# Performance work log

Measured on AMD Instinct MI355X. Metric: run time of the kernel, lower is better.

The kernel has to match this reference:

```python
import jax, jax.numpy as jnp
import numpy as np
import math

D = 1024
H = 16
B = 4
N = 2048


def setup_inputs() -> dict:
    key = jax.random.key(0)
    ks = jax.random.split(key, 10)
    scale_qkv = 0.01
    def kaiming_uniform(k, shape, scale):
        # attenuated_kaiming_uniform_: fan_in = shape[1], gain for leaky_relu a=sqrt(5)
        fan_in = shape[1]
        gain = math.sqrt(2.0 / (1 + 5.0))
        bound = math.sqrt(3.0) * gain * scale / math.sqrt(fan_in)
        return jax.random.uniform(k, shape, jnp.float32, -bound, bound)
    return {
        "x_q": jax.random.normal(ks[0], (B, N, D), jnp.float32),
        "x_kv": jax.random.normal(ks[1], (B, N, D), jnp.float32),
        "Wq": kaiming_uniform(ks[2], (D, D), scale_qkv),
        "bq": jnp.zeros((D,), jnp.float32),
        "Wk": kaiming_uniform(ks[3], (D, D), scale_qkv),
        "bk": jnp.zeros((D,), jnp.float32),
        "Wv": kaiming_uniform(ks[4], (D, D), scale_qkv),
        "bv": jnp.zeros((D,), jnp.float32),
        "Wo": kaiming_uniform(ks[5], (D, D), 1.0),
        "bo": jnp.zeros((D,), jnp.float32),
    }


def reference(x_q, x_kv, Wq, bq, Wk, bk, Wv, bv, Wo, bo):
    bs, n, d = x_q.shape
    hd = d // H  # head dim
    # torch Linear: y = x @ W^T + b
    q = x_q @ Wq.T + bq
    k = x_kv @ Wk.T + bk
    v = x_kv @ Wv.T + bv
    # reshape to [bs, H, n, hd]
    q = q.reshape(bs, n, H, hd).transpose(0, 2, 1, 3)
    k = k.reshape(bs, n, H, hd).transpose(0, 2, 1, 3)
    v = v.reshape(bs, n, H, hd).transpose(0, 2, 1, 3)
    scores = jnp.einsum("bhqd,bhkd->bhqk", q, k) / math.sqrt(hd)
    seq_ids = jnp.arange(n)
    causal = (seq_ids[None, :] <= seq_ids[:, None]).astype(scores.dtype)  # [n, n]
    scores = scores + (1.0 - causal) * -10000.0
    probs = jax.nn.softmax(scores, axis=-1)
    out = jnp.einsum("bhqk,bhkd->bhqd", probs, v)
    out = out.transpose(0, 2, 1, 3).reshape(bs, n, d)
    return out @ Wo.T + bo
```

## Files before the change

### kernel.cpp

```cpp
#include <hip/hip_runtime.h>

typedef unsigned short u16;
typedef unsigned int u32;
typedef __attribute__((ext_vector_type(8))) short short8;
typedef __attribute__((ext_vector_type(4))) float f32x4;
typedef __attribute__((ext_vector_type(16))) float f32x16;
typedef __attribute__((ext_vector_type(4))) unsigned u32x4;

#define ASYNC_CP16(gsrc, ldst) \
  __builtin_amdgcn_global_load_lds((__attribute__((address_space(1))) void*)(gsrc), \
                                   (__attribute__((address_space(3))) void*)(ldst), 16, 0, 0)

static __device__ __forceinline__ u16 f2bf(float f) {
  u32 u = __builtin_bit_cast(u32, f);
  u = u + 0x7fffu + ((u >> 16) & 1u);
  return (u16)(u >> 16);
}
static __device__ __forceinline__ u32 pk2(float a, float b) {
  return (u32)f2bf(a) | ((u32)f2bf(b) << 16);
}
static __device__ __forceinline__ u32 cvtpk(float lo, float hi) {
  u32 r;
  asm("v_cvt_pk_bf16_f32 %0, %1, %2" : "=v"(r) : "v"(lo), "v"(hi));
  return r;
}
static __device__ __forceinline__ void plswap(u32 &a, u32 &b) {
  asm("v_permlane32_swap_b32 %0, %1" : "+v"(a), "+v"(b));
}

__global__ __launch_bounds__(256) void convert_all(
    const float* __restrict__ xq, const float* __restrict__ xkv,
    const float* __restrict__ wq, const float* __restrict__ wk,
    const float* __restrict__ wv, const float* __restrict__ wo,
    u16* __restrict__ dst)
{
  long i = ((long)blockIdx.x * 256 + threadIdx.x) * 4;
  const float* s; long o;
  if      (i < 8388608)  { s = xq;  o = i; }
  else if (i < 16777216) { s = xkv; o = i - 8388608; }
  else if (i < 17825792) { s = wq;  o = i - 16777216; }
  else if (i < 18874368) { s = wk;  o = i - 17825792; }
  else if (i < 19922944) { s = wv;  o = i - 18874368; }
  else                   { s = wo;  o = i - 19922944; }
  float4 v = *(const float4*)(s + o);
  uint2 pkv; pkv.x = pk2(v.x, v.y); pkv.y = pk2(v.z, v.w);
  *(uint2*)(dst + i) = pkv;
}

template<int EPI>
__global__ __launch_bounds__(256)
void gemm_k(const u16* __restrict__ Axq, const u16* __restrict__ Axkv,
            const u16* __restrict__ W0, const u16* __restrict__ W1, const u16* __restrict__ W2,
            const float* __restrict__ b0, const float* __restrict__ b1, const float* __restrict__ b2,
            u16* __restrict__ Qo, u16* __restrict__ Ko, u16* __restrict__ Vo,
            float* __restrict__ Fo)
{
  __shared__ u16 lsa[2][128*32];
  __shared__ u16 lsb[2][128*32];
  const int tid = threadIdx.x;
  const int w = tid >> 6, lane = tid & 63;
  const int wr = w >> 1, wc = w & 1;
  const int bm = blockIdx.x, bn = blockIdx.y, z = blockIdx.z;
  const int l15 = lane & 15, l4 = lane >> 4;

  const u16* A; const u16* W; const float* bias;
  if (EPI == 0) {
    A    = (z == 0) ? Axq : Axkv;
    W    = (z == 0) ? W0 : (z == 1) ? W1 : W2;
    bias = (z == 0) ? b0 : (z == 1) ? b1 : b2;
  } else {
    A = Axq; W = W0; bias = b0;
  }
  const u16* Ag = A + (long)bm*128*1024;
  const u16* Wg = W + (long)bn*128*1024;

  f32x4 acc[4][4];
#pragma unroll
  for (int i = 0; i < 4; ++i)
#pragma unroll
    for (int j = 0; j < 4; ++j)
      acc[i][j] = (f32x4){0.f,0.f,0.f,0.f};

#pragma unroll
  for (int c = 0; c < 2; ++c) {
    int tp = c*256 + tid;
    int row = tp >> 2, col = (tp & 3) * 8;
    ASYNC_CP16(Ag + (long)row*1024 + col, &lsa[0][tp*8]);
    ASYNC_CP16(Wg + (long)row*1024 + col, &lsb[0][tp*8]);
  }

  for (int t = 0; t < 32; ++t) {
    const int cur = t & 1;
    if (t < 31) {
      const int k0 = (t + 1) * 32;
#pragma unroll
      for (int c = 0; c < 2; ++c) {
        int tp = c*256 + tid;
        int row = tp >> 2, col = (tp & 3) * 8;
        ASYNC_CP16(Ag + (long)row*1024 + k0 + col, &lsa[cur^1][tp*8]);
        ASYNC_CP16(Wg + (long)row*1024 + k0 + col, &lsb[cur^1][tp*8]);
      }
      asm volatile("s_waitcnt vmcnt(4)" ::: "memory");
    } else {
      asm volatile("s_waitcnt vmcnt(0)" ::: "memory");
    }
    __builtin_amdgcn_s_barrier();

    short8 af[4], bfr[4];
#pragma unroll
    for (int i = 0; i < 4; ++i)
      af[i] = *(const short8*)&lsa[cur][(wr*64 + i*16 + l15)*32 + l4*8];
#pragma unroll
    for (int j = 0; j < 4; ++j)
      bfr[j] = *(const short8*)&lsb[cur][(wc*64 + j*16 + l15)*32 + l4*8];
#pragma unroll
    for (int i = 0; i < 4; ++i)
#pragma unroll
      for (int j = 0; j < 4; ++j)
        acc[i][j] = __builtin_amdgcn_mfma_f32_16x16x32_bf16(af[i], bfr[j], acc[i][j], 0, 0, 0);

    asm volatile("" ::: "memory");
    __builtin_amdgcn_s_barrier();
  }

#pragma unroll
  for (int j = 0; j < 4; ++j) {
    const int colg = bn*128 + wc*64 + j*16 + l15;
    const float bb = bias[colg];
#pragma unroll
    for (int i = 0; i < 4; ++i) {
      const int rowg = bm*128 + wr*64 + i*16 + l4*4;
      if (EPI == 1) {
#pragma unroll
        for (int r = 0; r < 4; ++r)
          Fo[(long)(rowg + r)*1024 + colg] = acc[i][j][r] + bb;
      } else {
        const int b  = rowg >> 11, n0 = rowg & 2047;
        const int h  = colg >> 6,  c  = colg & 63;
        const int bh = b*16 + h;
        const long hb = (long)bh*131072 + (long)(n0 >> 7)*8192;
        if (z == 0) {
#pragma unroll
          for (int r = 0; r < 4; ++r)
            Qo[((long)bh*2048 + n0 + r)*64 + c] = f2bf((acc[i][j][r] + bb) * 0.18033688f);
        } else if (z == 1) {
          const long base = hb + (long)(c >> 3)*1024 + (n0 & 127)*8 + (c & 7);
#pragma unroll
          for (int r = 0; r < 4; ++r)
            Ko[base + r*8] = f2bf(acc[i][j][r] + bb);
        } else {
          const long base = hb + (long)((n0 & 127) >> 3)*512 + (long)c*8 + (n0 & 7);
          uint2 pkv;
          pkv.x = pk2(acc[i][j][0] + bb, acc[i][j][1] + bb);
          pkv.y = pk2(acc[i][j][2] + bb, acc[i][j][3] + bb);
          *(uint2*)(Vo + base) = pkv;
        }
      }
    }
  }
}

__global__ __launch_bounds__(512, 4)
void attn_k(const u16* __restrict__ Q, const u16* __restrict__ K,
            const u16* __restrict__ V, u16* __restrict__ AO)
{
  __shared__ u16 lk[2][8192];
  __shared__ u16 lv[2][8192];
  const int tid = threadIdx.x;
  const int w = tid >> 6, lane = tid & 63;
  const int l31 = lane & 31, l5 = lane >> 5;
  const int wq = w & 3, hh = w >> 2;
  const int qt = (gridDim.x - 1) - blockIdx.x;
  const int bh = blockIdx.y;
  const int q0 = qt*128;
  const int qg = q0 + wq*32 + l31;
  const u16* Qh = Q + (long)bh*131072;
  const u16* Kh = K + (long)bh*131072;
  const u16* Vh = V + (long)bh*131072;

  short8 qf[4];
#pragma unroll
  for (int ks = 0; ks < 4; ++ks)
    qf[ks] = *(const short8*)&Qh[(long)qg*64 + ks*16 + l5*8];

  f32x16 o0 = (f32x16)0.0f;
  f32x16 o1 = (f32x16)0.0f;
  float rsum = 0.f;

  const int koff = l5*2048 + l31*16;
  const int voff = l5*1024 + l31*16;
  const int ktmax = qt;

#pragma unroll
  for (int c = 0; c < 2; ++c) {
    int tp = c*512 + tid;
    ASYNC_CP16(Kh + tp*8, &lk[0][tp*8]);
    ASYNC_CP16(Vh + tp*8, &lv[0][tp*8]);
  }

  for (int kt = 0; kt <= ktmax; ++kt) {
    const int cur = kt & 1;
    if (kt < ktmax) {
      const long off = (long)(kt + 1)*8192;
#pragma unroll
      for (int c = 0; c < 2; ++c) {
        int tp = c*512 + tid;
        ASYNC_CP16(Kh + off + tp*8, &lk[cur^1][tp*8]);
        ASYNC_CP16(Vh + off + tp*8, &lv[cur^1][tp*8]);
      }
      asm volatile("s_waitcnt vmcnt(4)" ::: "memory");
    } else {
      asm volatile("s_waitcnt vmcnt(0)" ::: "memory");
    }
    __builtin_amdgcn_s_barrier();

    const char* lkc = (const char*)lk + cur*16384;
    const char* lvc = (const char*)lv + cur*16384;

    const bool active = !(kt == ktmax && hh*64 > wq*32 + 31);
    if (active) {
      short8 pf[4];
#pragma unroll
      for (int sbl = 0; sbl < 2; ++sbl) {
        f32x16 sa = (f32x16)0.0f;
#pragma unroll
        for (int ks = 0; ks < 4; ++ks) {
          short8 kf = *(const short8*)(lkc + koff + ks*4096 + (hh*2 + sbl)*512);
          sa = __builtin_amdgcn_mfma_f32_32x32x16_bf16(kf, qf[ks], sa, 0, 0, 0);
        }
        if (kt == ktmax) {
          const int kb = kt*128 + hh*64 + sbl*32 + 4*l5;
#pragma unroll
          for (int g = 0; g < 4; ++g)
#pragma unroll
            for (int rr = 0; rr < 4; ++rr)
              if (kb + 8*g + rr > qg) sa[4*g + rr] = -1e30f;
        }
        float p[16];
#pragma unroll
        for (int r = 0; r < 16; ++r) p[r] = __builtin_amdgcn_exp2f(sa[r]);
#pragma unroll
        for (int g = 0; g < 4; ++g)
          rsum += (p[4*g] + p[4*g+1]) + (p[4*g+2] + p[4*g+3]);
        u32 cc[4][2];
#pragma unroll
        for (int g = 0; g < 4; ++g) {
          cc[g][0] = cvtpk(p[4*g],   p[4*g+1]);
          cc[g][1] = cvtpk(p[4*g+2], p[4*g+3]);
        }
        plswap(cc[0][0], cc[1][0]); plswap(cc[0][1], cc[1][1]);
        plswap(cc[2][0], cc[3][0]); plswap(cc[2][1], cc[3][1]);
        u32x4 pw0 = {cc[0][0], cc[0][1], cc[1][0], cc[1][1]};
        u32x4 pw1 = {cc[2][0], cc[2][1], cc[3][0], cc[3][1]};
        pf[sbl*2]     = __builtin_bit_cast(short8, pw0);
        pf[sbl*2 + 1] = __builtin_bit_cast(short8, pw1);
      }
#pragma unroll
      for (int j = 0; j < 4; ++j) {
        const char* vb = lvc + voff + (hh*4 + j)*2048;
        short8 vf0 = *(const short8*)(vb);
        o0 = __builtin_amdgcn_mfma_f32_32x32x16_bf16(vf0, pf[j], o0, 0, 0, 0);
        short8 vf1 = *(const short8*)(vb + 512);
        o1 = __builtin_amdgcn_mfma_f32_32x32x16_bf16(vf1, pf[j], o1, 0, 0, 0);
      }
    }

    asm volatile("" ::: "memory");
    __builtin_amdgcn_s_barrier();
  }

  __syncthreads();
  float* exf = (float*)&lk[0][0];
  float* rxf = (float*)&lv[0][0];
  const int sw = lane & 7;
  float* xb = exf + wq*2048 + lane*32;

  if (hh == 1) {
#pragma unroll
    for (int c = 0; c < 4; ++c) {
      f32x4 v; v[0]=o0[c*4]; v[1]=o0[c*4+1]; v[2]=o0[c*4+2]; v[3]=o0[c*4+3];
      *(f32x4*)(xb + ((c ^ sw)*4)) = v;
    }
#pragma unroll
    for (int c = 0; c < 4; ++c) {
      f32x4 v; v[0]=o1[c*4]; v[1]=o1[c*4+1]; v[2]=o1[c*4+2]; v[3]=o1[c*4+3];
      *(f32x4*)(xb + (((c+4) ^ sw)*4)) = v;
    }
    rxf[wq*64 + lane] = rsum;
  }
  __syncthreads();
  if (hh == 0) {
    float rt = rsum + rxf[wq*64 + lane];
    rt += __shfl_xor(rt, 32, 64);
    const float inv = 1.0f / rt;
#pragma unroll
    for (int c = 0; c < 4; ++c) {
      f32x4 v = *(const f32x4*)(xb + ((c ^ sw)*4));
      o0[c*4] += v[0]; o0[c*4+1] += v[1]; o0[c*4+2] += v[2]; o0[c*4+3] += v[3];
    }
#pragma unroll
    for (int c = 0; c < 4; ++c) {
      f32x4 v = *(const f32x4*)(xb + (((c+4) ^ sw)*4));
      o1[c*4] += v[0]; o1[c*4+1] += v[1]; o1[c*4+2] += v[2]; o1[c*4+3] += v[3];
    }
    const int b = bh >> 4, h = bh & 15;
    const long tok = (long)b*2048 + qg;
    u16* dst = AO + tok*1024 + h*64;
#pragma unroll
    for (int g = 0; g < 4; ++g) {
      uint2 pkv;
      pkv.x = pk2(o0[4*g]*inv,   o0[4*g+1]*inv);
      pkv.y = pk2(o0[4*g+2]*inv, o0[4*g+3]*inv);
      *(uint2*)(dst + 8*g + 4*l5) = pkv;
    }
#pragma unroll
    for (int g = 0; g < 4; ++g) {
      uint2 pkv;
      pkv.x = pk2(o1[4*g]*inv,   o1[4*g+1]*inv);
      pkv.y = pk2(o1[4*g+2]*inv, o1[4*g+3]*inv);
      *(uint2*)(dst + 32 + 8*g + 4*l5) = pkv;
    }
  }
}

extern "C" void kernel_launch(void* const* d_in, const int* in_sizes, int n_in,
                              void* d_out, int out_size, void* d_ws, size_t ws_size,
                              hipStream_t stream)
{
  const float* xq  = (const float*)d_in[0];
  const float* xkv = (const float*)d_in[1];
  const float* Wq  = (const float*)d_in[2];
  const float* bq  = (const float*)d_in[3];
  const float* Wk  = (const float*)d_in[4];
  const float* bk  = (const float*)d_in[5];
  const float* Wv  = (const float*)d_in[6];
  const float* bv  = (const float*)d_in[7];
  const float* Wo  = (const float*)d_in[8];
  const float* bo  = (const float*)d_in[9];

  u16* ws    = (u16*)d_ws;
  u16* xq_b  = ws;
  u16* xkv_b = xq_b  + (1l<<23);
  u16* wq_b  = xkv_b + (1l<<23);
  u16* wk_b  = wq_b  + (1l<<20);
  u16* wv_b  = wk_b  + (1l<<20);
  u16* wo_b  = wv_b  + (1l<<20);
  u16* Qb    = wo_b  + (1l<<20);
  u16* Kb    = Qb    + (1l<<23);
  u16* Vb    = Kb    + (1l<<23);
  u16* Ab    = Vb    + (1l<<23);

  convert_all<<<20480, 256, 0, stream>>>(xq, xkv, Wq, Wk, Wv, Wo, ws);
  gemm_k<0><<<dim3(64,8,3), 256, 0, stream>>>(xq_b, xkv_b, wq_b, wk_b, wv_b,
                                              bq, bk, bv, Qb, Kb, Vb, nullptr);
  attn_k<<<dim3(16,64), 512, 0, stream>>>(Qb, Kb, Vb, Ab);
  gemm_k<1><<<dim3(64,8,1), 256, 0, stream>>>(Ab, nullptr, wo_b, nullptr, nullptr,
                                              bo, nullptr, nullptr,
                                              nullptr, nullptr, nullptr,
                                              (float*)d_out);
}
```

Before: 309.9 us.

## Rewrite projection GEMMs with 256x256 tiles, XOR-swizzled LDS, and priority scheduling

The QKV and output projection GEMMs now use 512-thread blocks computing 256x256 output tiles with a K step of 64 instead of 128x128 tiles with a K step of 32. The LDS layout is XOR-swizzled to avoid bank conflicts. MFMA bursts are interleaved with barriers and s_setprio to overlap loads with compute. This raises data reuse per global load and cuts the number of loop iterations. In exchange it launches fewer blocks (384 for QKV, 128 for the output GEMM), which may underfill the GPU, and it uses 128 KB of LDS per block.

```diff
diff --git a/kernel.cpp b/kernel.cpp
--- a/kernel.cpp
+++ b/kernel.cpp
@@ -48,18 +48,17 @@
 }
 
 template<int EPI>
-__global__ __launch_bounds__(256)
-void gemm_k(const u16* __restrict__ Axq, const u16* __restrict__ Axkv,
-            const u16* __restrict__ W0, const u16* __restrict__ W1, const u16* __restrict__ W2,
-            const float* __restrict__ b0, const float* __restrict__ b1, const float* __restrict__ b2,
-            u16* __restrict__ Qo, u16* __restrict__ Ko, u16* __restrict__ Vo,
-            float* __restrict__ Fo)
+__global__ __launch_bounds__(512, 2)
+void gemm8(const u16* __restrict__ Axq, const u16* __restrict__ Axkv,
+           const u16* __restrict__ W0, const u16* __restrict__ W1, const u16* __restrict__ W2,
+           const float* __restrict__ b0, const float* __restrict__ b1, const float* __restrict__ b2,
+           u16* __restrict__ Qo, u16* __restrict__ Ko, u16* __restrict__ Vo,
+           float* __restrict__ Fo)
 {
-  __shared__ u16 lsa[2][128*32];
-  __shared__ u16 lsb[2][128*32];
+  __shared__ u16 lds[65536];
   const int tid = threadIdx.x;
   const int w = tid >> 6, lane = tid & 63;
-  const int wr = w >> 1, wc = w & 1;
+  const int wm = w >> 2, wn = w & 3;
   const int bm = blockIdx.x, bn = blockIdx.y, z = blockIdx.z;
   const int l15 = lane & 15, l4 = lane >> 4;
 
@@ -71,69 +70,104 @@
   } else {
     A = Axq; W = W0; bias = b0;
   }
-  const u16* Ag = A + (long)bm*128*1024;
-  const u16* Wg = W + (long)bn*128*1024;
-
-  f32x4 acc[4][4];
-#pragma unroll
-  for (int i = 0; i < 4; ++i)
+  const u16* Ag = A + (long)bm*256*1024;
+  const u16* Wg = W + (long)bn*256*1024;
+
+  int srco[2][2], dsto[2][2];
+#pragma unroll
+  for (int h = 0; h < 2; ++h)
+#pragma unroll
+    for (int c = 0; c < 2; ++c) {
+      const int rowl = (c*512 + tid) >> 3;
+      const int kch  = (tid & 7) ^ (rowl & 7);
+      srco[h][c] = (h*128 + rowl)*1024 + kch*8;
+      dsto[h][c] = h*8192 + c*4096 + tid*8;
+    }
+
+  f32x4 acc[8][4];
+#pragma unroll
+  for (int i = 0; i < 8; ++i)
 #pragma unroll
     for (int j = 0; j < 4; ++j)
       acc[i][j] = (f32x4){0.f,0.f,0.f,0.f};
 
 #pragma unroll
-  for (int c = 0; c < 2; ++c) {
-    int tp = c*256 + tid;
-    int row = tp >> 2, col = (tp & 3) * 8;
-    ASYNC_CP16(Ag + (long)row*1024 + col, &lsa[0][tp*8]);
-    ASYNC_CP16(Wg + (long)row*1024 + col, &lsb[0][tp*8]);
-  }
-
-  for (int t = 0; t < 32; ++t) {
+  for (int h = 0; h < 2; ++h)
+#pragma unroll
+    for (int c = 0; c < 2; ++c) {
+      ASYNC_CP16(Ag + srco[h][c], &lds[dsto[h][c]]);
+      ASYNC_CP16(Wg + srco[h][c], &lds[32768 + dsto[h][c]]);
+    }
+  asm volatile("s_waitcnt vmcnt(0)" ::: "memory");
+  __builtin_amdgcn_s_barrier();
+
+  const int sx0 = ((l4)     ^ (l15 & 7)) * 8;
+  const int sx1 = ((4 + l4) ^ (l15 & 7)) * 8;
+
+  for (int t = 0; t < 16; ++t) {
     const int cur = t & 1;
-    if (t < 31) {
-      const int k0 = (t + 1) * 32;
-#pragma unroll
-      for (int c = 0; c < 2; ++c) {
-        int tp = c*256 + tid;
-        int row = tp >> 2, col = (tp & 3) * 8;
-        ASYNC_CP16(Ag + (long)row*1024 + k0 + col, &lsa[cur^1][tp*8]);
-        ASYNC_CP16(Wg + (long)row*1024 + k0 + col, &lsb[cur^1][tp*8]);
-      }
-      asm volatile("s_waitcnt vmcnt(4)" ::: "memory");
-    } else {
-      asm volatile("s_waitcnt vmcnt(0)" ::: "memory");
-    }
-    __builtin_amdgcn_s_barrier();
-
-    short8 af[4], bfr[4];
-#pragma unroll
-    for (int i = 0; i < 4; ++i)
-      af[i] = *(const short8*)&lsa[cur][(wr*64 + i*16 + l15)*32 + l4*8];
-#pragma unroll
-    for (int j = 0; j < 4; ++j)
-      bfr[j] = *(const short8*)&lsb[cur][(wc*64 + j*16 + l15)*32 + l4*8];
-#pragma unroll
-    for (int i = 0; i < 4; ++i)
-#pragma unroll
-      for (int j = 0; j < 4; ++j)
-        acc[i][j] = __builtin_amdgcn_mfma_f32_16x16x32_bf16(af[i], bfr[j], acc[i][j], 0, 0, 0);
-
-    asm volatile("" ::: "memory");
-    __builtin_amdgcn_s_barrier();
-  }
-
-#pragma unroll
-  for (int j = 0; j < 4; ++j) {
-    const int colg = bn*128 + wc*64 + j*16 + l15;
+    const u16* la = &lds[cur*16384];
+    const u16* lb = &lds[32768 + cur*16384];
+
+    if (t < 15) {
+      const int k0 = (t + 1)*64;
+      u16* da = &lds[(cur^1)*16384];
+      u16* db = &lds[32768 + (cur^1)*16384];
+#pragma unroll
+      for (int h = 0; h < 2; ++h)
+#pragma unroll
+        for (int c = 0; c < 2; ++c) {
+          ASYNC_CP16(Ag + srco[h][c] + k0, da + dsto[h][c]);
+          ASYNC_CP16(Wg + srco[h][c] + k0, db + dsto[h][c]);
+        }
+    }
+    short8 bfr[4][2];
+#pragma unroll
+    for (int fn = 0; fn < 4; ++fn) {
+      const u16* rb = lb + (wn*64 + fn*16 + l15)*64;
+      bfr[fn][0] = *(const short8*)(rb + sx0);
+      bfr[fn][1] = *(const short8*)(rb + sx1);
+    }
+
+#pragma unroll
+    for (int q = 0; q < 4; ++q) {
+      short8 af[2][2];
+#pragma unroll
+      for (int i = 0; i < 2; ++i) {
+        const u16* ra = la + (wm*128 + (q*2 + i)*16 + l15)*64;
+        af[i][0] = *(const short8*)(ra + sx0);
+        af[i][1] = *(const short8*)(ra + sx1);
+      }
+      __builtin_amdgcn_s_barrier();
+      asm volatile("s_waitcnt lgkmcnt(0)" ::: "memory");
+      __builtin_amdgcn_sched_barrier(0);
+      __builtin_amdgcn_s_setprio(1);
+#pragma unroll
+      for (int i = 0; i < 2; ++i)
+#pragma unroll
+        for (int fn = 0; fn < 4; ++fn) {
+          acc[q*2+i][fn] = __builtin_amdgcn_mfma_f32_16x16x32_bf16(af[i][0], bfr[fn][0], acc[q*2+i][fn], 0, 0, 0);
+          acc[q*2+i][fn] = __builtin_amdgcn_mfma_f32_16x16x32_bf16(af[i][1], bfr[fn][1], acc[q*2+i][fn], 0, 0, 0);
+        }
+      __builtin_amdgcn_s_setprio(0);
+      __builtin_amdgcn_sched_barrier(0);
+      if (q == 3 && t < 15)
+        asm volatile("s_waitcnt vmcnt(0)" ::: "memory");
+      __builtin_amdgcn_s_barrier();
+    }
+  }
+
+#pragma unroll
+  for (int fn = 0; fn < 4; ++fn) {
+    const int colg = bn*256 + wn*64 + fn*16 + l15;
     const float bb = bias[colg];
 #pragma unroll
-    for (int i = 0; i < 4; ++i) {
-      const int rowg = bm*128 + wr*64 + i*16 + l4*4;
+    for (int fm = 0; fm < 8; ++fm) {
+      const int rowg = bm*256 + wm*128 + fm*16 + l4*4;
       if (EPI == 1) {
 #pragma unroll
         for (int r = 0; r < 4; ++r)
-          Fo[(long)(rowg + r)*1024 + colg] = acc[i][j][r] + bb;
+          Fo[(long)(rowg + r)*1024 + colg] = acc[fm][fn][r] + bb;
       } else {
         const int b  = rowg >> 11, n0 = rowg & 2047;
         const int h  = colg >> 6,  c  = colg & 63;
@@ -142,17 +176,17 @@
         if (z == 0) {
 #pragma unroll
           for (int r = 0; r < 4; ++r)
-            Qo[((long)bh*2048 + n0 + r)*64 + c] = f2bf((acc[i][j][r] + bb) * 0.18033688f);
+            Qo[((long)bh*2048 + n0 + r)*64 + c] = f2bf((acc[fm][fn][r] + bb) * 0.18033688f);
         } else if (z == 1) {
           const long base = hb + (long)(c >> 3)*1024 + (n0 & 127)*8 + (c & 7);
 #pragma unroll
           for (int r = 0; r < 4; ++r)
-            Ko[base + r*8] = f2bf(acc[i][j][r] + bb);
+            Ko[base + r*8] = f2bf(acc[fm][fn][r] + bb);
         } else {
           const long base = hb + (long)((n0 & 127) >> 3)*512 + (long)c*8 + (n0 & 7);
           uint2 pkv;
-          pkv.x = pk2(acc[i][j][0] + bb, acc[i][j][1] + bb);
-          pkv.y = pk2(acc[i][j][2] + bb, acc[i][j][3] + bb);
+          pkv.x = pk2(acc[fm][fn][0] + bb, acc[fm][fn][1] + bb);
+          pkv.y = pk2(acc[fm][fn][2] + bb, acc[fm][fn][3] + bb);
           *(uint2*)(Vo + base) = pkv;
         }
       }
@@ -351,11 +385,11 @@
   u16* Ab    = Vb    + (1l<<23);
 
   convert_all<<<20480, 256, 0, stream>>>(xq, xkv, Wq, Wk, Wv, Wo, ws);
-  gemm_k<0><<<dim3(64,8,3), 256, 0, stream>>>(xq_b, xkv_b, wq_b, wk_b, wv_b,
-                                              bq, bk, bv, Qb, Kb, Vb, nullptr);
+  gemm8<0><<<dim3(32,4,3), 512, 0, stream>>>(xq_b, xkv_b, wq_b, wk_b, wv_b,
+                                             bq, bk, bv, Qb, Kb, Vb, nullptr);
   attn_k<<<dim3(16,64), 512, 0, stream>>>(Qb, Kb, Vb, Ab);
-  gemm_k<1><<<dim3(64,8,1), 256, 0, stream>>>(Ab, nullptr, wo_b, nullptr, nullptr,
-                                              bo, nullptr, nullptr,
-                                              nullptr, nullptr, nullptr,
-                                              (float*)d_out);
-}
+  gemm8<1><<<dim3(32,4,1), 512, 0, stream>>>(Ab, nullptr, wo_b, nullptr, nullptr,
+                                             bo, nullptr, nullptr,
+                                             nullptr, nullptr, nullptr,
+                                             (float*)d_out);
+}
```

After: 310.8 us. Within noise of the previous version (+0.3%).

## Split QKV projection into Q GEMM and fused K/V GEMM sharing the x_kv tile

Applied to the files above, without the earlier changes.

Replaces the single templated three-way (z-indexed) projection GEMM with a dedicated Q GEMM, a combined K/V GEMM, and a separate output GEMM. The K/V kernel loads each x_kv tile once into LDS and multiplies it against both the Wk and Wv tiles, holding two accumulator sets. This removes the duplicate A-tile loads and removes per-block branching on z. The trade-off is a K/V kernel with twice the accumulator registers and 1.5x the LDS (launch_bounds 256,2), which may reduce occupancy, and an extra kernel launch.

```diff
diff --git a/kernel.cpp b/kernel.cpp
--- a/kernel.cpp
+++ b/kernel.cpp
@@ -47,30 +47,18 @@
   *(uint2*)(dst + i) = pkv;
 }
 
-template<int EPI>
 __global__ __launch_bounds__(256)
-void gemm_k(const u16* __restrict__ Axq, const u16* __restrict__ Axkv,
-            const u16* __restrict__ W0, const u16* __restrict__ W1, const u16* __restrict__ W2,
-            const float* __restrict__ b0, const float* __restrict__ b1, const float* __restrict__ b2,
-            u16* __restrict__ Qo, u16* __restrict__ Ko, u16* __restrict__ Vo,
-            float* __restrict__ Fo)
+void gemm_q(const u16* __restrict__ A, const u16* __restrict__ W,
+            const float* __restrict__ bias, u16* __restrict__ Qo)
 {
   __shared__ u16 lsa[2][128*32];
   __shared__ u16 lsb[2][128*32];
   const int tid = threadIdx.x;
   const int w = tid >> 6, lane = tid & 63;
   const int wr = w >> 1, wc = w & 1;
-  const int bm = blockIdx.x, bn = blockIdx.y, z = blockIdx.z;
+  const int bm = blockIdx.x, bn = blockIdx.y;
   const int l15 = lane & 15, l4 = lane >> 4;
 
-  const u16* A; const u16* W; const float* bias;
-  if (EPI == 0) {
-    A    = (z == 0) ? Axq : Axkv;
-    W    = (z == 0) ? W0 : (z == 1) ? W1 : W2;
-    bias = (z == 0) ? b0 : (z == 1) ? b1 : b2;
-  } else {
-    A = Axq; W = W0; bias = b0;
-  }
   const u16* Ag = A + (long)bm*128*1024;
   const u16* Wg = W + (long)bn*128*1024;
 
@@ -127,35 +115,194 @@
   for (int j = 0; j < 4; ++j) {
     const int colg = bn*128 + wc*64 + j*16 + l15;
     const float bb = bias[colg];
+    const int h = colg >> 6, c = colg & 63;
 #pragma unroll
     for (int i = 0; i < 4; ++i) {
       const int rowg = bm*128 + wr*64 + i*16 + l4*4;
-      if (EPI == 1) {
-#pragma unroll
-        for (int r = 0; r < 4; ++r)
-          Fo[(long)(rowg + r)*1024 + colg] = acc[i][j][r] + bb;
-      } else {
-        const int b  = rowg >> 11, n0 = rowg & 2047;
-        const int h  = colg >> 6,  c  = colg & 63;
-        const int bh = b*16 + h;
-        const long hb = (long)bh*131072 + (long)(n0 >> 7)*8192;
-        if (z == 0) {
-#pragma unroll
-          for (int r = 0; r < 4; ++r)
-            Qo[((long)bh*2048 + n0 + r)*64 + c] = f2bf((acc[i][j][r] + bb) * 0.18033688f);
-        } else if (z == 1) {
-          const long base = hb + (long)(c >> 3)*1024 + (n0 & 127)*8 + (c & 7);
-#pragma unroll
-          for (int r = 0; r < 4; ++r)
-            Ko[base + r*8] = f2bf(acc[i][j][r] + bb);
-        } else {
-          const long base = hb + (long)((n0 & 127) >> 3)*512 + (long)c*8 + (n0 & 7);
-          uint2 pkv;
-          pkv.x = pk2(acc[i][j][0] + bb, acc[i][j][1] + bb);
-          pkv.y = pk2(acc[i][j][2] + bb, acc[i][j][3] + bb);
-          *(uint2*)(Vo + base) = pkv;
-        }
-      }
+      const int b = rowg >> 11, n0 = rowg & 2047;
+      const int bh = b*16 + h;
+#pragma unroll
+      for (int r = 0; r < 4; ++r)
+        Qo[((long)bh*2048 + n0 + r)*64 + c] = f2bf((acc[i][j][r] + bb) * 0.18033688f);
+    }
+  }
+}
+
+__global__ __launch_bounds__(256, 2)
+void gemm_kv(const u16* __restrict__ A, const u16* __restrict__ Wk,
+             const u16* __restrict__ Wv,
+             const float* __restrict__ bkb, const float* __restrict__ bvb,
+             u16* __restrict__ Ko, u16* __restrict__ Vo)
+{
+  __shared__ u16 lsa[2][128*32];
+  __shared__ u16 lsk[2][128*32];
+  __shared__ u16 lsv[2][128*32];
+  const int tid = threadIdx.x;
+  const int w = tid >> 6, lane = tid & 63;
+  const int wr = w >> 1, wc = w & 1;
+  const int bm = blockIdx.x, bn = blockIdx.y;
+  const int l15 = lane & 15, l4 = lane >> 4;
+
+  const u16* Ag = A  + (long)bm*128*1024;
+  const u16* Kg = Wk + (long)bn*128*1024;
+  const u16* Vg = Wv + (long)bn*128*1024;
+
+  f32x4 ak[4][4], av[4][4];
+#pragma unroll
+  for (int i = 0; i < 4; ++i)
+#pragma unroll
+    for (int j = 0; j < 4; ++j) {
+      ak[i][j] = (f32x4){0.f,0.f,0.f,0.f};
+      av[i][j] = (f32x4){0.f,0.f,0.f,0.f};
+    }
+
+#pragma unroll
+  for (int c = 0; c < 2; ++c) {
+    int tp = c*256 + tid;
+    int row = tp >> 2, col = (tp & 3) * 8;
+    ASYNC_CP16(Ag + (long)row*1024 + col, &lsa[0][tp*8]);
+    ASYNC_CP16(Kg + (long)row*1024 + col, &lsk[0][tp*8]);
+    ASYNC_CP16(Vg + (long)row*1024 + col, &lsv[0][tp*8]);
+  }
+
+  for (int t = 0; t < 32; ++t) {
+    const int cur = t & 1;
+    if (t < 31) {
+      const int k0 = (t + 1) * 32;
+#pragma unroll
+      for (int c = 0; c < 2; ++c) {
+        int tp = c*256 + tid;
+        int row = tp >> 2, col = (tp & 3) * 8;
+        ASYNC_CP16(Ag + (long)row*1024 + k0 + col, &lsa[cur^1][tp*8]);
+        ASYNC_CP16(Kg + (long)row*1024 + k0 + col, &lsk[cur^1][tp*8]);
+        ASYNC_CP16(Vg + (long)row*1024 + k0 + col, &lsv[cur^1][tp*8]);
+      }
+      asm volatile("s_waitcnt vmcnt(6)" ::: "memory");
+    } else {
+      asm volatile("s_waitcnt vmcnt(0)" ::: "memory");
+    }
+    __builtin_amdgcn_s_barrier();
+
+    short8 af[4], kf[4], vf[4];
+#pragma unroll
+    for (int i = 0; i < 4; ++i)
+      af[i] = *(const short8*)&lsa[cur][(wr*64 + i*16 + l15)*32 + l4*8];
+#pragma unroll
+    for (int j = 0; j < 4; ++j) {
+      kf[j] = *(const short8*)&lsk[cur][(wc*64 + j*16 + l15)*32 + l4*8];
+      vf[j] = *(const short8*)&lsv[cur][(wc*64 + j*16 + l15)*32 + l4*8];
+    }
+#pragma unroll
+    for (int i = 0; i < 4; ++i)
+#pragma unroll
+      for (int j = 0; j < 4; ++j) {
+        ak[i][j] = __builtin_amdgcn_mfma_f32_16x16x32_bf16(af[i], kf[j], ak[i][j], 0, 0, 0);
+        av[i][j] = __builtin_amdgcn_mfma_f32_16x16x32_bf16(af[i], vf[j], av[i][j], 0, 0, 0);
+      }
+
+    asm volatile("" ::: "memory");
+    __builtin_amdgcn_s_barrier();
+  }
+
+#pragma unroll
+  for (int j = 0; j < 4; ++j) {
+    const int colg = bn*128 + wc*64 + j*16 + l15;
+    const float kb = bkb[colg];
+    const float vb = bvb[colg];
+    const int h = colg >> 6, c = colg & 63;
+#pragma unroll
+    for (int i = 0; i < 4; ++i) {
+      const int rowg = bm*128 + wr*64 + i*16 + l4*4;
+      const int b = rowg >> 11, n0 = rowg & 2047;
+      const int bh = b*16 + h;
+      const long hb = (long)bh*131072 + (long)(n0 >> 7)*8192;
+      const long kbase = hb + (long)(c >> 3)*1024 + (n0 & 127)*8 + (c & 7);
+#pragma unroll
+      for (int r = 0; r < 4; ++r)
+        Ko[kbase + r*8] = f2bf(ak[i][j][r] + kb);
+      const long vbase = hb + (long)((n0 & 127) >> 3)*512 + (long)c*8 + (n0 & 7);
+      uint2 pkv;
+      pkv.x = pk2(av[i][j][0] + vb, av[i][j][1] + vb);
+      pkv.y = pk2(av[i][j][2] + vb, av[i][j][3] + vb);
+      *(uint2*)(Vo + vbase) = pkv;
+    }
+  }
+}
+
+__global__ __launch_bounds__(256)
+void gemm_o(const u16* __restrict__ A, const u16* __restrict__ W,
+            const float* __restrict__ bias, float* __restrict__ Fo)
+{
+  __shared__ u16 lsa[2][128*32];
+  __shared__ u16 lsb[2][128*32];
+  const int tid = threadIdx.x;
+  const int w = tid >> 6, lane = tid & 63;
+  const int wr = w >> 1, wc = w & 1;
+  const int bm = blockIdx.x, bn = blockIdx.y;
+  const int l15 = lane & 15, l4 = lane >> 4;
+
+  const u16* Ag = A + (long)bm*128*1024;
+  const u16* Wg = W + (long)bn*128*1024;
+
+  f32x4 acc[4][4];
+#pragma unroll
+  for (int i = 0; i < 4; ++i)
+#pragma unroll
+    for (int j = 0; j < 4; ++j)
+      acc[i][j] = (f32x4){0.f,0.f,0.f,0.f};
+
+#pragma unroll
+  for (int c = 0; c < 2; ++c) {
+    int tp = c*256 + tid;
+    int row = tp >> 2, col = (tp & 3) * 8;
+    ASYNC_CP16(Ag + (long)row*1024 + col, &lsa[0][tp*8]);
+    ASYNC_CP16(Wg + (long)row*1024 + col, &lsb[0][tp*8]);
+  }
+
+  for (int t = 0; t < 32; ++t) {
+    const int cur = t & 1;
+    if (t < 31) {
+      const int k0 = (t + 1) * 32;
+#pragma unroll
+      for (int c = 0; c < 2; ++c) {
+        int tp = c*256 + tid;
+        int row = tp >> 2, col = (tp & 3) * 8;
+        ASYNC_CP16(Ag + (long)row*1024 + k0 + col, &lsa[cur^1][tp*8]);
+        ASYNC_CP16(Wg + (long)row*1024 + k0 + col, &lsb[cur^1][tp*8]);
+      }
+      asm volatile("s_waitcnt vmcnt(4)" ::: "memory");
+    } else {
+      asm volatile("s_waitcnt vmcnt(0)" ::: "memory");
+    }
+    __builtin_amdgcn_s_barrier();
+
+    short8 af[4], bfr[4];
+#pragma unroll
+    for (int i = 0; i < 4; ++i)
+      af[i] = *(const short8*)&lsa[cur][(wr*64 + i*16 + l15)*32 + l4*8];
+#pragma unroll
+    for (int j = 0; j < 4; ++j)
+      bfr[j] = *(const short8*)&lsb[cur][(wc*64 + j*16 + l15)*32 + l4*8];
+#pragma unroll
+    for (int i = 0; i < 4; ++i)
+#pragma unroll
+      for (int j = 0; j < 4; ++j)
+        acc[i][j] = __builtin_amdgcn_mfma_f32_16x16x32_bf16(af[i], bfr[j], acc[i][j], 0, 0, 0);
+
+    asm volatile("" ::: "memory");
+    __builtin_amdgcn_s_barrier();
+  }
+
+#pragma unroll
+  for (int j = 0; j < 4; ++j) {
+    const int colg = bn*128 + wc*64 + j*16 + l15;
+    const float bb = bias[colg];
+#pragma unroll
+    for (int i = 0; i < 4; ++i) {
+      const int rowg = bm*128 + wr*64 + i*16 + l4*4;
+#pragma unroll
+      for (int r = 0; r < 4; ++r)
+        Fo[(long)(rowg + r)*1024 + colg] = acc[i][j][r] + bb;
     }
   }
 }
@@ -351,11 +498,8 @@
   u16* Ab    = Vb    + (1l<<23);
 
   convert_all<<<20480, 256, 0, stream>>>(xq, xkv, Wq, Wk, Wv, Wo, ws);
-  gemm_k<0><<<dim3(64,8,3), 256, 0, stream>>>(xq_b, xkv_b, wq_b, wk_b, wv_b,
-                                              bq, bk, bv, Qb, Kb, Vb, nullptr);
+  gemm_q<<<dim3(64,8), 256, 0, stream>>>(xq_b, wq_b, bq, Qb);
+  gemm_kv<<<dim3(64,8), 256, 0, stream>>>(xkv_b, wk_b, wv_b, bk, bv, Kb, Vb);
   attn_k<<<dim3(16,64), 512, 0, stream>>>(Qb, Kb, Vb, Ab);
-  gemm_k<1><<<dim3(64,8,1), 256, 0, stream>>>(Ab, nullptr, wo_b, nullptr, nullptr,
-                                              bo, nullptr, nullptr,
-                                              nullptr, nullptr, nullptr,
-                                              (float*)d_out);
-}
+  gemm_o<<<dim3(64,8), 256, 0, stream>>>(Ab, wo_b, bo, (float*)d_out);
+}
```

New measurement: 302.4 us. -2.4%, faster.
